# Kernel tuning notes

Measured on AMD Instinct MI355X. Metric: run time of the kernel, lower is better.

Reference implementation:

```python
import jax, jax.numpy as jnp
import numpy as np

N, E, H, D = 4096, 512, 8, 64
SCALE = np.sqrt(D).astype(np.float32)

def setup_inputs() -> dict:
    key = jax.random.key(0)
    ks = jax.random.split(key, 9)
    s = 1.0 / np.sqrt(E)
    return {
        'x':  jax.random.normal(ks[0], (N, E), dtype=jnp.float32),
        'Wq': jax.random.normal(ks[1], (E, E), dtype=jnp.float32) * s,
        'bq': jax.random.normal(ks[2], (E,), dtype=jnp.float32) * s,
        'Wk': jax.random.normal(ks[3], (E, E), dtype=jnp.float32) * s,
        'bk': jax.random.normal(ks[4], (E,), dtype=jnp.float32) * s,
        'Wv': jax.random.normal(ks[5], (E, E), dtype=jnp.float32) * s,
        'bv': jax.random.normal(ks[6], (E,), dtype=jnp.float32) * s,
        'Wo': jax.random.normal(ks[7], (E, E), dtype=jnp.float32) * s,
        'bo': jax.random.normal(ks[8], (E,), dtype=jnp.float32) * s,
    }

def reference(x, Wq, bq, Wk, bk, Wv, bv, Wo, bo):
    n = x.shape[0]
    # Linear layers (torch Linear: y = x @ W.T + b)
    Q = (x @ Wq.T + bq).reshape(n, H, D)  # [N,H,D]
    K = (x @ Wk.T + bk).reshape(n, H, D)
    V = (x @ Wv.T + bv).reshape(n, H, D)
    # scores over the batch axis: [H,N,N]
    scores = jnp.einsum('nhd,mhd->hnm', Q, K) / SCALE
    attn = jax.nn.softmax(scores, axis=-1)  # [H,N,N]
    ctx = jnp.einsum('hnm,mhd->nhd', attn, V).reshape(n, E)
    out = ctx @ Wo.T + bo  # [N,E]
    return out, attn, Q, K, V
```

## Files before the change

### kernel.cpp

```cpp
#include <hip/hip_runtime.h>
#include <hip/hip_bf16.h>
#include <math.h>

#define TOK   4096
#define EDIM  512
#define HEADS 8
#define DHEAD 64

typedef __attribute__((ext_vector_type(8))) short short8v;
typedef __attribute__((ext_vector_type(4))) float float4v;
typedef __attribute__((ext_vector_type(4))) unsigned int uint4v;

#define SC2 0.180336880111f

__device__ __forceinline__ unsigned short f2bf(float f) {
    unsigned int u = __float_as_uint(f);
    unsigned int r = (u + 0x7FFFu + ((u >> 16) & 1u)) >> 16;
    return (unsigned short)r;
}
__device__ __forceinline__ unsigned int packbf_tr(float lo, float hi) {
    return __builtin_amdgcn_perm(__float_as_uint(hi), __float_as_uint(lo), 0x07060302u);
}
__device__ __forceinline__ float fast_exp2(float x) {
#if __has_builtin(__builtin_amdgcn_exp2f)
    return __builtin_amdgcn_exp2f(x);
#else
    return __expf(x * 0.69314718f);
#endif
}

__global__ __launch_bounds__(256) void to_bf16_all(
    const float* __restrict__ x,
    const float* __restrict__ wq, const float* __restrict__ wk,
    const float* __restrict__ wv, const float* __restrict__ wo,
    unsigned short* __restrict__ xb,
    unsigned short* __restrict__ wqb, unsigned short* __restrict__ wkb,
    unsigned short* __restrict__ wvb, unsigned short* __restrict__ wob)
{
    const int bid = blockIdx.x;
    const float* src; unsigned short* dst; int idx;
    if (bid < 1024) { src = x; dst = xb; idx = bid; }
    else {
        const int k = (bid - 1024) >> 7;
        idx = (bid - 1024) & 127;
        src = (k == 0) ? wq : (k == 1) ? wk : (k == 2) ? wv : wo;
        dst = (k == 0) ? wqb : (k == 1) ? wkb : (k == 2) ? wvb : wob;
    }
    const int off = idx * 2048 + threadIdx.x * 8;
    float4 a = *(const float4*)(src + off);
    float4 b = *(const float4*)(src + off + 4);
    short8v o;
    o[0] = (short)f2bf(a.x); o[1] = (short)f2bf(a.y);
    o[2] = (short)f2bf(a.z); o[3] = (short)f2bf(a.w);
    o[4] = (short)f2bf(b.x); o[5] = (short)f2bf(b.y);
    o[6] = (short)f2bf(b.z); o[7] = (short)f2bf(b.w);
    *(short8v*)(dst + off) = o;
}

template<int MODE>
__global__ __launch_bounds__(256, 3) void gemm512(
    const unsigned short* __restrict__ A,
    const unsigned short* __restrict__ W,
    const float* __restrict__ bias,
    float* __restrict__ Y,
    unsigned short* __restrict__ sec)
{
    __shared__ alignas(16) char sA[2][8192];
    __shared__ alignas(16) char sB[2][8192];

    const int t = threadIdx.x;
    const int lane = t & 63, w = t >> 6;
    const int l15 = lane & 15, g4 = lane >> 4;
    const int wr = w >> 1, wc = w & 1;
    const int m0 = blockIdx.y * 64, n0 = blockIdx.x * 64;

    short8v areg[2], breg[2];

#define GL(kk) { _Pragma("unroll") for (int j = 0; j < 2; ++j) { \
        const int unit_ = j * 256 + t, row_ = unit_ >> 3, u_ = unit_ & 7; \
        areg[j] = *(const short8v*)(A + (size_t)(m0 + row_) * 512 + (kk) * 64 + u_ * 8); \
        breg[j] = *(const short8v*)(W + (size_t)(n0 + row_) * 512 + (kk) * 64 + u_ * 8); } }
#define GW(b) { _Pragma("unroll") for (int j = 0; j < 2; ++j) { \
        const int unit_ = j * 256 + t, row_ = unit_ >> 3, u_ = unit_ & 7; \
        const int byt_ = row_ * 128 + ((u_ ^ (row_ & 7)) * 16); \
        *(short8v*)(sA[b] + byt_) = areg[j]; *(short8v*)(sB[b] + byt_) = breg[j]; } }

    float4v acc[2][2];
#pragma unroll
    for (int mi = 0; mi < 2; ++mi)
#pragma unroll
        for (int ni = 0; ni < 2; ++ni) acc[mi][ni] = (float4v){0.f, 0.f, 0.f, 0.f};

    GL(0); GW(0); __syncthreads();

#pragma unroll 2
    for (int kk = 0; kk < 8; ++kk) {
        if (kk < 7) GL(kk + 1);
        const char* cA = sA[kk & 1];
        const char* cB = sB[kk & 1];
        short8v af[2][2], bf[2][2];
#pragma unroll
        for (int mi = 0; mi < 2; ++mi)
#pragma unroll
            for (int kh = 0; kh < 2; ++kh) {
                const int row = wr * 32 + mi * 16 + l15;
                af[mi][kh] = *(const short8v*)(cA + row * 128 + (((kh * 4 + g4) ^ (l15 & 7)) * 16));
            }
#pragma unroll
        for (int ni = 0; ni < 2; ++ni)
#pragma unroll
            for (int kh = 0; kh < 2; ++kh) {
                const int row = wc * 32 + ni * 16 + l15;
                bf[ni][kh] = *(const short8v*)(cB + row * 128 + (((kh * 4 + g4) ^ (l15 & 7)) * 16));
            }
        __builtin_amdgcn_s_setprio(1);
#pragma unroll
        for (int mi = 0; mi < 2; ++mi)
#pragma unroll
            for (int ni = 0; ni < 2; ++ni) {
                acc[mi][ni] = __builtin_amdgcn_mfma_f32_16x16x32_bf16(af[mi][0], bf[ni][0], acc[mi][ni], 0, 0, 0);
                acc[mi][ni] = __builtin_amdgcn_mfma_f32_16x16x32_bf16(af[mi][1], bf[ni][1], acc[mi][ni], 0, 0, 0);
            }
        __builtin_amdgcn_s_setprio(0);
        if (kk < 7) GW((kk + 1) & 1);
        __syncthreads();
    }

#pragma unroll
    for (int mi = 0; mi < 2; ++mi)
#pragma unroll
        for (int ni = 0; ni < 2; ++ni) {
            const int col = n0 + wc * 32 + ni * 16 + l15;
            const float bb = bias[col];
#pragma unroll
            for (int r = 0; r < 4; ++r) {
                const int row = m0 + wr * 32 + mi * 16 + g4 * 4 + r;
                const float v = acc[mi][ni][r] + bb;
                Y[(size_t)row * 512 + col] = v;
                if (MODE == 1)
                    sec[((size_t)(col >> 6) * TOK + row) * 64 + (col & 63)] = f2bf(v);
                if (MODE == 2)
                    sec[((size_t)(col >> 6) * 64 + (col & 63)) * TOK + row] = f2bf(v);
            }
        }
#undef GL
#undef GW
}

__global__ __launch_bounds__(256, 3) void fused_attn(
    const float* __restrict__ Q,
    const unsigned short* __restrict__ Kb,
    const unsigned short* __restrict__ Vt,
    float* __restrict__ attn,
    unsigned short* __restrict__ ctxb)
{
    __shared__ alignas(16) char lds[32768];

    const int t = threadIdx.x;
    const int lane = t & 63, w = t >> 6;
    const int l15 = lane & 15, g4 = lane >> 4;
    const int bid = blockIdx.x;
    const int h = bid & 7;
    const int n0 = (bid >> 3) * 64;
    const int nw = n0 + w * 16;

    const unsigned short* KbH = Kb + (size_t)h * TOK * DHEAD;
    const unsigned short* VtH = Vt + (size_t)h * DHEAD * TOK;

    short8v bq[2];
    {
        const float* qp = Q + (size_t)(nw + l15) * EDIM + h * DHEAD + g4 * 8;
#pragma unroll
        for (int ks = 0; ks < 2; ++ks) {
            float4 u = *(const float4*)(qp + ks * 32);
            float4 v = *(const float4*)(qp + ks * 32 + 4);
            bq[ks][0] = (short)f2bf(u.x); bq[ks][1] = (short)f2bf(u.y);
            bq[ks][2] = (short)f2bf(u.z); bq[ks][3] = (short)f2bf(u.w);
            bq[ks][4] = (short)f2bf(v.x); bq[ks][5] = (short)f2bf(v.y);
            bq[ks][6] = (short)f2bf(v.z); bq[ks][7] = (short)f2bf(v.w);
        }
    }

    short8v kreg[4], vreg[4];
#define LK(c) { _Pragma("unroll") for (int j = 0; j < 4; ++j) { \
        const int unit_ = j * 256 + t, row_ = unit_ >> 3, u_ = unit_ & 7; \
        kreg[j] = *(const short8v*)(KbH + (size_t)((c) * 128 + row_) * 64 + u_ * 8); } }
#define WK1(b) { _Pragma("unroll") for (int j = 0; j < 4; ++j) { \
        const int unit_ = j * 256 + t, row_ = unit_ >> 3, u_ = unit_ & 7; \
        *(short8v*)(lds + (b) * 16384 + row_ * 128 + ((u_ ^ (row_ & 7)) * 16)) = kreg[j]; } }
#define WK2() { _Pragma("unroll") for (int j = 0; j < 4; ++j) { \
        const int unit_ = j * 256 + t, row_ = unit_ >> 3, u_ = unit_ & 7; \
        *(short8v*)(lds + row_ * 128 + ((u_ ^ (row_ & 7)) * 16)) = kreg[j]; } }
#define LV(c) { _Pragma("unroll") for (int j = 0; j < 4; ++j) { \
        const int unit_ = j * 256 + t, row_ = unit_ >> 4, u_ = unit_ & 15; \
        vreg[j] = *(const short8v*)(VtH + (size_t)row_ * TOK + (c) * 128 + u_ * 8); } }
#define WV() { _Pragma("unroll") for (int j = 0; j < 4; ++j) { \
        const int unit_ = j * 256 + t, row_ = unit_ >> 4, u_ = unit_ & 15; \
        *(short8v*)(lds + 16384 + row_ * 256 + ((u_ ^ (row_ & 7)) * 16)) = vreg[j]; } }

    float p4[4] = {0.f, 0.f, 0.f, 0.f};

    LK(0); WK1(0); __syncthreads();
#pragma unroll 2
    for (int c = 0; c < 32; ++c) {
        if (c < 31) LK(c + 1);
        const char* sKc = lds + (c & 1) * 16384;
#pragma unroll
        for (int mt = 0; mt < 8; ++mt) {
            const int row = mt * 16 + l15;
            short8v k0 = *(const short8v*)(sKc + row * 128 + ((g4 ^ (l15 & 7)) * 16));
            short8v k1 = *(const short8v*)(sKc + row * 128 + (((4 + g4) ^ (l15 & 7)) * 16));
            __builtin_amdgcn_s_setprio(1);
            float4v s = (float4v){0.f, 0.f, 0.f, 0.f};
            s = __builtin_amdgcn_mfma_f32_16x16x32_bf16(k0, bq[0], s, 0, 0, 0);
            s = __builtin_amdgcn_mfma_f32_16x16x32_bf16(k1, bq[1], s, 0, 0, 0);
            __builtin_amdgcn_s_setprio(0);
#pragma unroll
            for (int r = 0; r < 4; ++r)
                p4[r] += fast_exp2(s[r] * SC2);
        }
        if (c < 31) WK1((c + 1) & 1);
        __syncthreads();
    }

    float srun = (p4[0] + p4[1]) + (p4[2] + p4[3]);
#pragma unroll
    for (int off = 16; off <= 32; off <<= 1)
        srun += __shfl_xor(srun, off, 64);
    const float inv = 1.0f / srun;

    float* attnH = attn + ((size_t)h * TOK + nw) * TOK;
    float4v cacc[4];
#pragma unroll
    for (int dt = 0; dt < 4; ++dt) cacc[dt] = (float4v){0.f, 0.f, 0.f, 0.f};

    LK(0); LV(0); WK2(); WV(); __syncthreads();
    for (int c = 0; c < 32; ++c) {
        if (c < 31) { LK(c + 1); LV(c + 1); }
        const int mbase = c * 128;
        unsigned int u[8][2];
#pragma unroll
        for (int mt = 0; mt < 8; ++mt) {
            const int row = mt * 16 + l15;
            short8v k0 = *(const short8v*)(lds + row * 128 + ((g4 ^ (l15 & 7)) * 16));
            short8v k1 = *(const short8v*)(lds + row * 128 + (((4 + g4) ^ (l15 & 7)) * 16));
            __builtin_amdgcn_s_setprio(1);
            float4v s = (float4v){0.f, 0.f, 0.f, 0.f};
            s = __builtin_amdgcn_mfma_f32_16x16x32_bf16(k0, bq[0], s, 0, 0, 0);
            s = __builtin_amdgcn_mfma_f32_16x16x32_bf16(k1, bq[1], s, 0, 0, 0);
            __builtin_amdgcn_s_setprio(0);
            float4v p;
#pragma unroll
            for (int r = 0; r < 4; ++r)
                p[r] = fast_exp2(s[r] * SC2) * inv;
            __builtin_nontemporal_store(
                p, (float4v*)(attnH + (size_t)l15 * TOK + mbase + mt * 16 + g4 * 4));
            u[mt][0] = packbf_tr(p[0], p[1]);
            u[mt][1] = packbf_tr(p[2], p[3]);
        }
#pragma unroll
        for (int ks = 0; ks < 4; ++ks) {
            const int sA = l15 + ((lane & 16) << 1);
            const int sB = sA + 16;
            unsigned int lo0 = __shfl(u[2 * ks][0], sA, 64);
            unsigned int lo1 = __shfl(u[2 * ks][1], sA, 64);
            unsigned int lo2 = __shfl(u[2 * ks][0], sB, 64);
            unsigned int lo3 = __shfl(u[2 * ks][1], sB, 64);
            unsigned int hi0 = __shfl(u[2 * ks + 1][0], sA, 64);
            unsigned int hi1 = __shfl(u[2 * ks + 1][1], sA, 64);
            unsigned int hi2 = __shfl(u[2 * ks + 1][0], sB, 64);
            unsigned int hi3 = __shfl(u[2 * ks + 1][1], sB, 64);
            uint4v wv4;
            const bool sel = (lane & 32) != 0;
            wv4[0] = sel ? hi0 : lo0;
            wv4[1] = sel ? hi1 : lo1;
            wv4[2] = sel ? hi2 : lo2;
            wv4[3] = sel ? hi3 : lo3;
            const short8v pa = __builtin_bit_cast(short8v, wv4);
            __builtin_amdgcn_s_setprio(1);
#pragma unroll
            for (int dt = 0; dt < 4; ++dt) {
                const int rowv = dt * 16 + l15;
                short8v vf = *(const short8v*)(lds + 16384 + rowv * 256 + (((ks * 4 + g4) ^ (l15 & 7)) * 16));
                cacc[dt] = __builtin_amdgcn_mfma_f32_16x16x32_bf16(pa, vf, cacc[dt], 0, 0, 0);
            }
            __builtin_amdgcn_s_setprio(0);
        }
        __syncthreads();
        if (c < 31) { WK2(); WV(); __syncthreads(); }
    }

#pragma unroll
    for (int dt = 0; dt < 4; ++dt)
#pragma unroll
        for (int r = 0; r < 4; ++r)
            ctxb[(size_t)(nw + g4 * 4 + r) * EDIM + h * DHEAD + dt * 16 + l15] =
                f2bf(cacc[dt][r]);
#undef LK
#undef WK1
#undef WK2
#undef LV
#undef WV
}

extern "C" void kernel_launch(void* const* d_in, const int* in_sizes, int n_in,
                              void* d_out, int out_size, void* d_ws, size_t ws_size,
                              hipStream_t stream) {
    (void)in_sizes; (void)n_in; (void)out_size; (void)ws_size;

    const float* x  = (const float*)d_in[0];
    const float* Wq = (const float*)d_in[1];
    const float* bq = (const float*)d_in[2];
    const float* Wk = (const float*)d_in[3];
    const float* bk = (const float*)d_in[4];
    const float* Wv = (const float*)d_in[5];
    const float* bv = (const float*)d_in[6];
    const float* Wo = (const float*)d_in[7];
    const float* bo = (const float*)d_in[8];

    float* out  = (float*)d_out;
    float* attn = out  + (size_t)TOK * EDIM;
    float* Qf   = attn + (size_t)HEADS * TOK * TOK;
    float* Kf   = Qf   + (size_t)TOK * EDIM;
    float* Vf   = Kf   + (size_t)TOK * EDIM;

    char* wsb = (char*)d_ws;
    unsigned short* xb   = (unsigned short*)wsb;
    unsigned short* wqb  = (unsigned short*)(wsb + (4u << 20));
    unsigned short* wkb  = (unsigned short*)(wsb + (4u << 20) + (512u << 10));
    unsigned short* wvb  = (unsigned short*)(wsb + (5u << 20));
    unsigned short* wob  = (unsigned short*)(wsb + (5u << 20) + (512u << 10));
    unsigned short* KbW  = (unsigned short*)(wsb + (6u << 20));
    unsigned short* VtW  = (unsigned short*)(wsb + (10u << 20));
    unsigned short* ctxb = xb;

    to_bf16_all<<<1536, 256, 0, stream>>>(x, Wq, Wk, Wv, Wo, xb, wqb, wkb, wvb, wob);

    dim3 gg(EDIM / 64, TOK / 64);
    gemm512<0><<<gg, 256, 0, stream>>>(xb, wqb, bq, Qf, nullptr);
    gemm512<1><<<gg, 256, 0, stream>>>(xb, wkb, bk, Kf, KbW);
    gemm512<2><<<gg, 256, 0, stream>>>(xb, wvb, bv, Vf, VtW);

    fused_attn<<<512, 256, 0, stream>>>(Qf, KbW, VtW, attn, ctxb);

    gemm512<0><<<gg, 256, 0, stream>>>(ctxb, wob, bo, out, nullptr);
}
```

Measured before the change: 240.0 us.

## Split attention key range across warps with register-held K/V and LDS reduction

Each warp now handles all 64 query rows of the block over its own quarter of the key range, instead of each warp owning 16 query rows and sweeping all keys. K and V are loaded straight from global memory into registers rather than staged through shared memory, which drops the per-chunk block barriers. Probabilities go through a per-warp LDS scratch to form the P operand instead of cross-lane shuffles. Row sums and the context partials are combined across warps in LDS at the end. The cost is more registers and more LDS (about 69KB), so launch bounds drop from 3 to 2 blocks per CU, which lowers occupancy, and the attn writes become strided per warp.

```diff
diff --git a/kernel.cpp b/kernel.cpp
--- a/kernel.cpp
+++ b/kernel.cpp
@@ -147,14 +147,15 @@
 #undef GW
 }
 
-__global__ __launch_bounds__(256, 3) void fused_attn(
+__global__ __launch_bounds__(256, 2) void fused_attn(
     const float* __restrict__ Q,
     const unsigned short* __restrict__ Kb,
     const unsigned short* __restrict__ Vt,
     float* __restrict__ attn,
     unsigned short* __restrict__ ctxb)
 {
-    __shared__ alignas(16) char lds[32768];
+    __shared__ alignas(16) char ldsbig[69632];
+    __shared__ float redS[256];
 
     const int t = threadIdx.x;
     const int lane = t & 63, w = t >> 6;
@@ -162,145 +163,157 @@
     const int bid = blockIdx.x;
     const int h = bid & 7;
     const int n0 = (bid >> 3) * 64;
-    const int nw = n0 + w * 16;
+    const int mw0 = w * 1024;
+    const int xsw = (l15 & 7) << 1;
 
     const unsigned short* KbH = Kb + (size_t)h * TOK * DHEAD;
     const unsigned short* VtH = Vt + (size_t)h * DHEAD * TOK;
-
-    short8v bq[2];
-    {
-        const float* qp = Q + (size_t)(nw + l15) * EDIM + h * DHEAD + g4 * 8;
+    char* myP = ldsbig + w * 8192;
+
+    short8v bq[4][2];
+#pragma unroll
+    for (int rg = 0; rg < 4; ++rg) {
+        const float* qp = Q + (size_t)(n0 + rg * 16 + l15) * EDIM + h * DHEAD + g4 * 8;
 #pragma unroll
         for (int ks = 0; ks < 2; ++ks) {
             float4 u = *(const float4*)(qp + ks * 32);
             float4 v = *(const float4*)(qp + ks * 32 + 4);
-            bq[ks][0] = (short)f2bf(u.x); bq[ks][1] = (short)f2bf(u.y);
-            bq[ks][2] = (short)f2bf(u.z); bq[ks][3] = (short)f2bf(u.w);
-            bq[ks][4] = (short)f2bf(v.x); bq[ks][5] = (short)f2bf(v.y);
-            bq[ks][6] = (short)f2bf(v.z); bq[ks][7] = (short)f2bf(v.w);
-        }
-    }
-
-    short8v kreg[4], vreg[4];
-#define LK(c) { _Pragma("unroll") for (int j = 0; j < 4; ++j) { \
-        const int unit_ = j * 256 + t, row_ = unit_ >> 3, u_ = unit_ & 7; \
-        kreg[j] = *(const short8v*)(KbH + (size_t)((c) * 128 + row_) * 64 + u_ * 8); } }
-#define WK1(b) { _Pragma("unroll") for (int j = 0; j < 4; ++j) { \
-        const int unit_ = j * 256 + t, row_ = unit_ >> 3, u_ = unit_ & 7; \
-        *(short8v*)(lds + (b) * 16384 + row_ * 128 + ((u_ ^ (row_ & 7)) * 16)) = kreg[j]; } }
-#define WK2() { _Pragma("unroll") for (int j = 0; j < 4; ++j) { \
-        const int unit_ = j * 256 + t, row_ = unit_ >> 3, u_ = unit_ & 7; \
-        *(short8v*)(lds + row_ * 128 + ((u_ ^ (row_ & 7)) * 16)) = kreg[j]; } }
-#define LV(c) { _Pragma("unroll") for (int j = 0; j < 4; ++j) { \
-        const int unit_ = j * 256 + t, row_ = unit_ >> 4, u_ = unit_ & 15; \
-        vreg[j] = *(const short8v*)(VtH + (size_t)row_ * TOK + (c) * 128 + u_ * 8); } }
-#define WV() { _Pragma("unroll") for (int j = 0; j < 4; ++j) { \
-        const int unit_ = j * 256 + t, row_ = unit_ >> 4, u_ = unit_ & 15; \
-        *(short8v*)(lds + 16384 + row_ * 256 + ((u_ ^ (row_ & 7)) * 16)) = vreg[j]; } }
+            bq[rg][ks][0] = (short)f2bf(u.x); bq[rg][ks][1] = (short)f2bf(u.y);
+            bq[rg][ks][2] = (short)f2bf(u.z); bq[rg][ks][3] = (short)f2bf(u.w);
+            bq[rg][ks][4] = (short)f2bf(v.x); bq[rg][ks][5] = (short)f2bf(v.y);
+            bq[rg][ks][6] = (short)f2bf(v.z); bq[rg][ks][7] = (short)f2bf(v.w);
+        }
+    }
+
+#define LOADK(b, c) { _Pragma("unroll") for (int mt_ = 0; mt_ < 4; ++mt_) \
+        _Pragma("unroll") for (int ks_ = 0; ks_ < 2; ++ks_) \
+        ka[b][mt_][ks_] = *(const short8v*)(KbH + \
+            (size_t)(mw0 + (c) * 64 + mt_ * 16 + l15) * 64 + ks_ * 32 + g4 * 8); }
 
     float p4[4] = {0.f, 0.f, 0.f, 0.f};
-
-    LK(0); WK1(0); __syncthreads();
+    {
+        short8v ka[2][4][2];
+        LOADK(0, 0)
 #pragma unroll 2
-    for (int c = 0; c < 32; ++c) {
-        if (c < 31) LK(c + 1);
-        const char* sKc = lds + (c & 1) * 16384;
-#pragma unroll
-        for (int mt = 0; mt < 8; ++mt) {
-            const int row = mt * 16 + l15;
-            short8v k0 = *(const short8v*)(sKc + row * 128 + ((g4 ^ (l15 & 7)) * 16));
-            short8v k1 = *(const short8v*)(sKc + row * 128 + (((4 + g4) ^ (l15 & 7)) * 16));
-            __builtin_amdgcn_s_setprio(1);
-            float4v s = (float4v){0.f, 0.f, 0.f, 0.f};
-            s = __builtin_amdgcn_mfma_f32_16x16x32_bf16(k0, bq[0], s, 0, 0, 0);
-            s = __builtin_amdgcn_mfma_f32_16x16x32_bf16(k1, bq[1], s, 0, 0, 0);
-            __builtin_amdgcn_s_setprio(0);
+        for (int c = 0; c < 16; ++c) {
+            const int cur = c & 1;
+            if (c < 15) LOADK(cur ^ 1, c + 1)
+#pragma unroll
+            for (int mt = 0; mt < 4; ++mt) {
+#pragma unroll
+                for (int rg = 0; rg < 4; ++rg) {
+                    float4v s = (float4v){0.f, 0.f, 0.f, 0.f};
+                    s = __builtin_amdgcn_mfma_f32_16x16x32_bf16(ka[cur][mt][0], bq[rg][0], s, 0, 0, 0);
+                    s = __builtin_amdgcn_mfma_f32_16x16x32_bf16(ka[cur][mt][1], bq[rg][1], s, 0, 0, 0);
+#pragma unroll
+                    for (int r = 0; r < 4; ++r)
+                        p4[rg] += fast_exp2(s[r] * SC2);
+                }
+            }
+        }
+    }
+#pragma unroll
+    for (int rg = 0; rg < 4; ++rg) {
+        p4[rg] += __shfl_xor(p4[rg], 16, 64);
+        p4[rg] += __shfl_xor(p4[rg], 32, 64);
+    }
+    if (lane < 16) {
+#pragma unroll
+        for (int rg = 0; rg < 4; ++rg)
+            redS[(rg * 16 + lane) * 4 + w] = p4[rg];
+    }
+    __syncthreads();
+    float inv[4];
+#pragma unroll
+    for (int rg = 0; rg < 4; ++rg) {
+        const float* rp = redS + (rg * 16 + l15) * 4;
+        inv[rg] = 1.0f / ((rp[0] + rp[1]) + (rp[2] + rp[3]));
+    }
+
+    float* aH[4];
+#pragma unroll
+    for (int rg = 0; rg < 4; ++rg)
+        aH[rg] = attn + ((size_t)h * TOK + n0 + rg * 16 + l15) * TOK;
+
+    float4v cacc[4][4];
+#pragma unroll
+    for (int ng = 0; ng < 4; ++ng)
+#pragma unroll
+        for (int dt = 0; dt < 4; ++dt) cacc[ng][dt] = (float4v){0.f, 0.f, 0.f, 0.f};
+
+    for (int c = 0; c < 16; ++c) {
+        const int mbase = mw0 + c * 64;
+        short8v vb[4][2];
+#pragma unroll
+        for (int dt = 0; dt < 4; ++dt)
+#pragma unroll
+            for (int ks2 = 0; ks2 < 2; ++ks2)
+                vb[dt][ks2] = *(const short8v*)(VtH + (size_t)(dt * 16 + l15) * TOK + mbase + ks2 * 32 + g4 * 8);
+        short8v ka[1][4][2];
+        LOADK(0, c)
+#pragma unroll
+        for (int mt = 0; mt < 4; ++mt) {
+#pragma unroll
+            for (int rg = 0; rg < 4; ++rg) {
+                float4v s = (float4v){0.f, 0.f, 0.f, 0.f};
+                s = __builtin_amdgcn_mfma_f32_16x16x32_bf16(ka[0][mt][0], bq[rg][0], s, 0, 0, 0);
+                s = __builtin_amdgcn_mfma_f32_16x16x32_bf16(ka[0][mt][1], bq[rg][1], s, 0, 0, 0);
+                float4v p;
+#pragma unroll
+                for (int r = 0; r < 4; ++r)
+                    p[r] = fast_exp2(s[r] * SC2) * inv[rg];
+                __builtin_nontemporal_store(
+                    p, (float4v*)(aH[rg] + mbase + mt * 16 + g4 * 4));
+                const unsigned int u0 = packbf_tr(p[0], p[1]);
+                const unsigned int u1 = packbf_tr(p[2], p[3]);
+                *(uint2*)(myP + (rg * 16 + l15) * 128 + (((mt * 4 + g4) ^ xsw) << 3)) =
+                    make_uint2(u0, u1);
+            }
+        }
+#pragma unroll
+        for (int ng = 0; ng < 4; ++ng) {
+#pragma unroll
+            for (int ks2 = 0; ks2 < 2; ++ks2) {
+                const uint4v pr = *(const uint4v*)(myP + (ng * 16 + l15) * 128 +
+                                                   (((ks2 * 8 + g4 * 2) ^ xsw) << 3));
+                const short8v pa = __builtin_bit_cast(short8v, pr);
+#pragma unroll
+                for (int dt = 0; dt < 4; ++dt)
+                    cacc[ng][dt] = __builtin_amdgcn_mfma_f32_16x16x32_bf16(pa, vb[dt][ks2], cacc[ng][dt], 0, 0, 0);
+            }
+        }
+    }
+#undef LOADK
+
+    __syncthreads();
+    float* osh = (float*)ldsbig + (size_t)w * 4352;
+#pragma unroll
+    for (int ng = 0; ng < 4; ++ng)
+#pragma unroll
+        for (int dt = 0; dt < 4; ++dt)
 #pragma unroll
             for (int r = 0; r < 4; ++r)
-                p4[r] += fast_exp2(s[r] * SC2);
-        }
-        if (c < 31) WK1((c + 1) & 1);
-        __syncthreads();
-    }
-
-    float srun = (p4[0] + p4[1]) + (p4[2] + p4[3]);
-#pragma unroll
-    for (int off = 16; off <= 32; off <<= 1)
-        srun += __shfl_xor(srun, off, 64);
-    const float inv = 1.0f / srun;
-
-    float* attnH = attn + ((size_t)h * TOK + nw) * TOK;
-    float4v cacc[4];
-#pragma unroll
-    for (int dt = 0; dt < 4; ++dt) cacc[dt] = (float4v){0.f, 0.f, 0.f, 0.f};
-
-    LK(0); LV(0); WK2(); WV(); __syncthreads();
-    for (int c = 0; c < 32; ++c) {
-        if (c < 31) { LK(c + 1); LV(c + 1); }
-        const int mbase = c * 128;
-        unsigned int u[8][2];
-#pragma unroll
-        for (int mt = 0; mt < 8; ++mt) {
-            const int row = mt * 16 + l15;
-            short8v k0 = *(const short8v*)(lds + row * 128 + ((g4 ^ (l15 & 7)) * 16));
-            short8v k1 = *(const short8v*)(lds + row * 128 + (((4 + g4) ^ (l15 & 7)) * 16));
-            __builtin_amdgcn_s_setprio(1);
-            float4v s = (float4v){0.f, 0.f, 0.f, 0.f};
-            s = __builtin_amdgcn_mfma_f32_16x16x32_bf16(k0, bq[0], s, 0, 0, 0);
-            s = __builtin_amdgcn_mfma_f32_16x16x32_bf16(k1, bq[1], s, 0, 0, 0);
-            __builtin_amdgcn_s_setprio(0);
-            float4v p;
-#pragma unroll
-            for (int r = 0; r < 4; ++r)
-                p[r] = fast_exp2(s[r] * SC2) * inv;
-            __builtin_nontemporal_store(
-                p, (float4v*)(attnH + (size_t)l15 * TOK + mbase + mt * 16 + g4 * 4));
-            u[mt][0] = packbf_tr(p[0], p[1]);
-            u[mt][1] = packbf_tr(p[2], p[3]);
-        }
-#pragma unroll
-        for (int ks = 0; ks < 4; ++ks) {
-            const int sA = l15 + ((lane & 16) << 1);
-            const int sB = sA + 16;
-            unsigned int lo0 = __shfl(u[2 * ks][0], sA, 64);
-            unsigned int lo1 = __shfl(u[2 * ks][1], sA, 64);
-            unsigned int lo2 = __shfl(u[2 * ks][0], sB, 64);
-            unsigned int lo3 = __shfl(u[2 * ks][1], sB, 64);
-            unsigned int hi0 = __shfl(u[2 * ks + 1][0], sA, 64);
-            unsigned int hi1 = __shfl(u[2 * ks + 1][1], sA, 64);
-            unsigned int hi2 = __shfl(u[2 * ks + 1][0], sB, 64);
-            unsigned int hi3 = __shfl(u[2 * ks + 1][1], sB, 64);
-            uint4v wv4;
-            const bool sel = (lane & 32) != 0;
-            wv4[0] = sel ? hi0 : lo0;
-            wv4[1] = sel ? hi1 : lo1;
-            wv4[2] = sel ? hi2 : lo2;
-            wv4[3] = sel ? hi3 : lo3;
-            const short8v pa = __builtin_bit_cast(short8v, wv4);
-            __builtin_amdgcn_s_setprio(1);
-#pragma unroll
-            for (int dt = 0; dt < 4; ++dt) {
-                const int rowv = dt * 16 + l15;
-                short8v vf = *(const short8v*)(lds + 16384 + rowv * 256 + (((ks * 4 + g4) ^ (l15 & 7)) * 16));
-                cacc[dt] = __builtin_amdgcn_mfma_f32_16x16x32_bf16(pa, vf, cacc[dt], 0, 0, 0);
-            }
-            __builtin_amdgcn_s_setprio(0);
-        }
-        __syncthreads();
-        if (c < 31) { WK2(); WV(); __syncthreads(); }
-    }
-
-#pragma unroll
-    for (int dt = 0; dt < 4; ++dt)
-#pragma unroll
-        for (int r = 0; r < 4; ++r)
-            ctxb[(size_t)(nw + g4 * 4 + r) * EDIM + h * DHEAD + dt * 16 + l15] =
-                f2bf(cacc[dt][r]);
-#undef LK
-#undef WK1
-#undef WK2
-#undef LV
-#undef WV
+                osh[(ng * 16 + g4 * 4 + r) * 68 + dt * 16 + l15] = cacc[ng][dt][r];
+    __syncthreads();
+    {
+        const int n = t >> 2, dq = t & 3;
+        const float* o0 = (const float*)ldsbig + n * 68 + dq * 16;
+        unsigned short ob[16];
+#pragma unroll
+        for (int q = 0; q < 4; ++q) {
+            float4 s = *(const float4*)(o0 + q * 4);
+#pragma unroll
+            for (int w2 = 1; w2 < 4; ++w2) {
+                const float4 a = *(const float4*)(o0 + (size_t)w2 * 4352 + q * 4);
+                s.x += a.x; s.y += a.y; s.z += a.z; s.w += a.w;
+            }
+            ob[q * 4 + 0] = f2bf(s.x); ob[q * 4 + 1] = f2bf(s.y);
+            ob[q * 4 + 2] = f2bf(s.z); ob[q * 4 + 3] = f2bf(s.w);
+        }
+        unsigned short* cp = ctxb + (size_t)(n0 + n) * EDIM + h * DHEAD + dq * 16;
+        *(short8v*)(cp)     = *(const short8v*)&ob[0];
+        *(short8v*)(cp + 8) = *(const short8v*)&ob[8];
+    }
 }
 
 extern "C" void kernel_launch(void* const* d_in, const int* in_sizes, int n_in,
```

New measurement: 294.5 us. 22.7% more time.

## Split attention key range across wave pairs with LDS P staging and reduction

Applied to the files above, without the earlier changes.

Each block now handles 32 query rows instead of 64, and pairs of waves split every 128-key chunk in half. Row sums and context partials are combined through LDS. The grid doubles to 1024 blocks and launch bounds rise to 4 blocks per CU, aiming for more occupancy and parallelism. The register shuffle transpose of P is replaced by staging through a per-wave swizzled LDS buffer. The attn store is no longer nontemporal, and each block loads K/V for half as many queries, which doubles total K/V traffic.

```diff
diff --git a/kernel.cpp b/kernel.cpp
--- a/kernel.cpp
+++ b/kernel.cpp
@@ -147,29 +147,34 @@
 #undef GW
 }
 
-__global__ __launch_bounds__(256, 3) void fused_attn(
+__global__ __launch_bounds__(256, 4) void fused_attn(
     const float* __restrict__ Q,
     const unsigned short* __restrict__ Kb,
     const unsigned short* __restrict__ Vt,
     float* __restrict__ attn,
     unsigned short* __restrict__ ctxb)
 {
-    __shared__ alignas(16) char lds[32768];
+    __shared__ alignas(16) char lds_main[32768];
+    __shared__ alignas(16) char ldsP[8192];
 
     const int t = threadIdx.x;
     const int lane = t & 63, w = t >> 6;
     const int l15 = lane & 15, g4 = lane >> 4;
     const int bid = blockIdx.x;
-    const int h = bid & 7;
-    const int n0 = (bid >> 3) * 64;
-    const int nw = n0 + w * 16;
+    const int h  = bid & 7;
+    const int n0 = (bid >> 3) * 32;
+    const int rg = w >> 1;
+    const int mh = w & 1;
+    const int xsw = (l15 & 7) << 1;
 
     const unsigned short* KbH = Kb + (size_t)h * TOK * DHEAD;
     const unsigned short* VtH = Vt + (size_t)h * DHEAD * TOK;
+    char* myP = ldsP + w * 2048;
+    float* redS = (float*)lds_main;
 
     short8v bq[2];
     {
-        const float* qp = Q + (size_t)(nw + l15) * EDIM + h * DHEAD + g4 * 8;
+        const float* qp = Q + (size_t)(n0 + rg * 16 + l15) * EDIM + h * DHEAD + g4 * 8;
 #pragma unroll
         for (int ks = 0; ks < 2; ++ks) {
             float4 u = *(const float4*)(qp + ks * 32);
@@ -185,29 +190,24 @@
 #define LK(c) { _Pragma("unroll") for (int j = 0; j < 4; ++j) { \
         const int unit_ = j * 256 + t, row_ = unit_ >> 3, u_ = unit_ & 7; \
         kreg[j] = *(const short8v*)(KbH + (size_t)((c) * 128 + row_) * 64 + u_ * 8); } }
-#define WK1(b) { _Pragma("unroll") for (int j = 0; j < 4; ++j) { \
+#define WK(base) { _Pragma("unroll") for (int j = 0; j < 4; ++j) { \
         const int unit_ = j * 256 + t, row_ = unit_ >> 3, u_ = unit_ & 7; \
-        *(short8v*)(lds + (b) * 16384 + row_ * 128 + ((u_ ^ (row_ & 7)) * 16)) = kreg[j]; } }
-#define WK2() { _Pragma("unroll") for (int j = 0; j < 4; ++j) { \
-        const int unit_ = j * 256 + t, row_ = unit_ >> 3, u_ = unit_ & 7; \
-        *(short8v*)(lds + row_ * 128 + ((u_ ^ (row_ & 7)) * 16)) = kreg[j]; } }
+        *(short8v*)((base) + row_ * 128 + ((u_ ^ (row_ & 7)) * 16)) = kreg[j]; } }
 #define LV(c) { _Pragma("unroll") for (int j = 0; j < 4; ++j) { \
         const int unit_ = j * 256 + t, row_ = unit_ >> 4, u_ = unit_ & 15; \
         vreg[j] = *(const short8v*)(VtH + (size_t)row_ * TOK + (c) * 128 + u_ * 8); } }
-#define WV() { _Pragma("unroll") for (int j = 0; j < 4; ++j) { \
+#define WV(base) { _Pragma("unroll") for (int j = 0; j < 4; ++j) { \
         const int unit_ = j * 256 + t, row_ = unit_ >> 4, u_ = unit_ & 15; \
-        *(short8v*)(lds + 16384 + row_ * 256 + ((u_ ^ (row_ & 7)) * 16)) = vreg[j]; } }
-
-    float p4[4] = {0.f, 0.f, 0.f, 0.f};
-
-    LK(0); WK1(0); __syncthreads();
-#pragma unroll 2
+        *(short8v*)((base) + row_ * 256 + ((u_ ^ (row_ & 7)) * 16)) = vreg[j]; } }
+
+    float psum = 0.f;
+    LK(0); WK(lds_main); __syncthreads();
     for (int c = 0; c < 32; ++c) {
         if (c < 31) LK(c + 1);
-        const char* sKc = lds + (c & 1) * 16384;
-#pragma unroll
-        for (int mt = 0; mt < 8; ++mt) {
-            const int row = mt * 16 + l15;
+        const char* sKc = lds_main + (c & 1) * 16384;
+#pragma unroll
+        for (int mt = 0; mt < 4; ++mt) {
+            const int row = mh * 64 + mt * 16 + l15;
             short8v k0 = *(const short8v*)(sKc + row * 128 + ((g4 ^ (l15 & 7)) * 16));
             short8v k1 = *(const short8v*)(sKc + row * 128 + (((4 + g4) ^ (l15 & 7)) * 16));
             __builtin_amdgcn_s_setprio(1);
@@ -217,33 +217,36 @@
             __builtin_amdgcn_s_setprio(0);
 #pragma unroll
             for (int r = 0; r < 4; ++r)
-                p4[r] += fast_exp2(s[r] * SC2);
-        }
-        if (c < 31) WK1((c + 1) & 1);
+                psum += fast_exp2(s[r] * SC2);
+        }
+        if (c < 31) WK(lds_main + ((c + 1) & 1) * 16384);
         __syncthreads();
     }
-
-    float srun = (p4[0] + p4[1]) + (p4[2] + p4[3]);
-#pragma unroll
-    for (int off = 16; off <= 32; off <<= 1)
-        srun += __shfl_xor(srun, off, 64);
-    const float inv = 1.0f / srun;
-
-    float* attnH = attn + ((size_t)h * TOK + nw) * TOK;
+    psum += __shfl_xor(psum, 16, 64);
+    psum += __shfl_xor(psum, 32, 64);
+    if (lane < 16)
+        redS[(rg * 16 + lane) * 2 + mh] = psum;
+    __syncthreads();
+    const float inv = 1.0f / (redS[(rg * 16 + l15) * 2] + redS[(rg * 16 + l15) * 2 + 1]);
+    __syncthreads();
+
+    float* aH = attn + ((size_t)h * TOK + n0 + rg * 16 + l15) * TOK;
     float4v cacc[4];
 #pragma unroll
     for (int dt = 0; dt < 4; ++dt) cacc[dt] = (float4v){0.f, 0.f, 0.f, 0.f};
 
-    LK(0); LV(0); WK2(); WV(); __syncthreads();
+    char* sK2 = lds_main;
+    char* sV2 = lds_main + 16384;
+
+    LK(0); LV(0); WK(sK2); WV(sV2); __syncthreads();
     for (int c = 0; c < 32; ++c) {
         if (c < 31) { LK(c + 1); LV(c + 1); }
-        const int mbase = c * 128;
-        unsigned int u[8][2];
-#pragma unroll
-        for (int mt = 0; mt < 8; ++mt) {
-            const int row = mt * 16 + l15;
-            short8v k0 = *(const short8v*)(lds + row * 128 + ((g4 ^ (l15 & 7)) * 16));
-            short8v k1 = *(const short8v*)(lds + row * 128 + (((4 + g4) ^ (l15 & 7)) * 16));
+        const int mbase = c * 128 + mh * 64;
+#pragma unroll
+        for (int mt = 0; mt < 4; ++mt) {
+            const int row = mh * 64 + mt * 16 + l15;
+            short8v k0 = *(const short8v*)(sK2 + row * 128 + ((g4 ^ (l15 & 7)) * 16));
+            short8v k1 = *(const short8v*)(sK2 + row * 128 + (((4 + g4) ^ (l15 & 7)) * 16));
             __builtin_amdgcn_s_setprio(1);
             float4v s = (float4v){0.f, 0.f, 0.f, 0.f};
             s = __builtin_amdgcn_mfma_f32_16x16x32_bf16(k0, bq[0], s, 0, 0, 0);
@@ -253,52 +256,56 @@
 #pragma unroll
             for (int r = 0; r < 4; ++r)
                 p[r] = fast_exp2(s[r] * SC2) * inv;
-            __builtin_nontemporal_store(
-                p, (float4v*)(attnH + (size_t)l15 * TOK + mbase + mt * 16 + g4 * 4));
-            u[mt][0] = packbf_tr(p[0], p[1]);
-            u[mt][1] = packbf_tr(p[2], p[3]);
-        }
-#pragma unroll
-        for (int ks = 0; ks < 4; ++ks) {
-            const int sA = l15 + ((lane & 16) << 1);
-            const int sB = sA + 16;
-            unsigned int lo0 = __shfl(u[2 * ks][0], sA, 64);
-            unsigned int lo1 = __shfl(u[2 * ks][1], sA, 64);
-            unsigned int lo2 = __shfl(u[2 * ks][0], sB, 64);
-            unsigned int lo3 = __shfl(u[2 * ks][1], sB, 64);
-            unsigned int hi0 = __shfl(u[2 * ks + 1][0], sA, 64);
-            unsigned int hi1 = __shfl(u[2 * ks + 1][1], sA, 64);
-            unsigned int hi2 = __shfl(u[2 * ks + 1][0], sB, 64);
-            unsigned int hi3 = __shfl(u[2 * ks + 1][1], sB, 64);
-            uint4v wv4;
-            const bool sel = (lane & 32) != 0;
-            wv4[0] = sel ? hi0 : lo0;
-            wv4[1] = sel ? hi1 : lo1;
-            wv4[2] = sel ? hi2 : lo2;
-            wv4[3] = sel ? hi3 : lo3;
-            const short8v pa = __builtin_bit_cast(short8v, wv4);
-            __builtin_amdgcn_s_setprio(1);
+            *(float4v*)(aH + mbase + mt * 16 + g4 * 4) = p;
+            const unsigned int u0 = packbf_tr(p[0], p[1]);
+            const unsigned int u1 = packbf_tr(p[2], p[3]);
+            *(uint2*)(myP + l15 * 128 + (((mt * 4 + g4) ^ xsw) << 3)) =
+                make_uint2(u0, u1);
+        }
+        __builtin_amdgcn_s_setprio(1);
+#pragma unroll
+        for (int ks2 = 0; ks2 < 2; ++ks2) {
+            const uint4v pr = *(const uint4v*)(myP + l15 * 128 +
+                                               (((ks2 * 8 + g4 * 2) ^ xsw) << 3));
+            const short8v pa = __builtin_bit_cast(short8v, pr);
 #pragma unroll
             for (int dt = 0; dt < 4; ++dt) {
                 const int rowv = dt * 16 + l15;
-                short8v vf = *(const short8v*)(lds + 16384 + rowv * 256 + (((ks * 4 + g4) ^ (l15 & 7)) * 16));
+                const int uu = (mh * 8 + ks2 * 4 + g4) ^ (l15 & 7);
+                short8v vf = *(const short8v*)(sV2 + rowv * 256 + uu * 16);
                 cacc[dt] = __builtin_amdgcn_mfma_f32_16x16x32_bf16(pa, vf, cacc[dt], 0, 0, 0);
             }
-            __builtin_amdgcn_s_setprio(0);
-        }
+        }
+        __builtin_amdgcn_s_setprio(0);
         __syncthreads();
-        if (c < 31) { WK2(); WV(); __syncthreads(); }
-    }
-
+        if (c < 31) { WK(sK2); WV(sV2); __syncthreads(); }
+    }
+
+    float* osh = (float*)lds_main + (size_t)w * 1088;
 #pragma unroll
     for (int dt = 0; dt < 4; ++dt)
 #pragma unroll
         for (int r = 0; r < 4; ++r)
-            ctxb[(size_t)(nw + g4 * 4 + r) * EDIM + h * DHEAD + dt * 16 + l15] =
-                f2bf(cacc[dt][r]);
+            osh[(g4 * 4 + r) * 68 + dt * 16 + l15] = cacc[dt][r];
+    __syncthreads();
+    {
+        const int n = t >> 3, dq = t & 7;
+        const int w0 = (n >> 4) * 2;
+        const float* o0 = (const float*)lds_main + (size_t)w0 * 1088 + (n & 15) * 68 + dq * 8;
+        unsigned short ob[8];
+#pragma unroll
+        for (int q = 0; q < 2; ++q) {
+            float4 s = *(const float4*)(o0 + q * 4);
+            const float4 a = *(const float4*)(o0 + 1088 + q * 4);
+            s.x += a.x; s.y += a.y; s.z += a.z; s.w += a.w;
+            ob[q * 4 + 0] = f2bf(s.x); ob[q * 4 + 1] = f2bf(s.y);
+            ob[q * 4 + 2] = f2bf(s.z); ob[q * 4 + 3] = f2bf(s.w);
+        }
+        *(short8v*)(ctxb + (size_t)(n0 + n) * EDIM + h * DHEAD + dq * 8) =
+            *(const short8v*)&ob[0];
+    }
 #undef LK
-#undef WK1
-#undef WK2
+#undef WK
 #undef LV
 #undef WV
 }
@@ -341,7 +348,7 @@
     gemm512<1><<<gg, 256, 0, stream>>>(xb, wkb, bk, Kf, KbW);
     gemm512<2><<<gg, 256, 0, stream>>>(xb, wvb, bv, Vf, VtW);
 
-    fused_attn<<<512, 256, 0, stream>>>(Qf, KbW, VtW, attn, ctxb);
+    fused_attn<<<1024, 256, 0, stream>>>(Qf, KbW, VtW, attn, ctxb);
 
     gemm512<0><<<gg, 256, 0, stream>>>(ctxb, wob, bo, out, nullptr);
 }
```

New measurement: 206.4 us. 1.16x faster.
